# Kernel optimization log

Hardware: AMD Instinct MI355X
Metric: run time of the kernel (lower is better)

## Reference

```python
import jax, jax.numpy as jnp
import numpy as np

NUM_GROUPS, GROUP_SIZE, D_MODEL = 8, 4096, 1024
NUM_EXPERTS = 64
EXPERT_CAPACITY = 1024  # capacity_factor 2: 2 * total_tokens / num_experts


def setup_inputs() -> dict:
    key = jax.random.key(0)
    k1, k2, k3 = jax.random.split(key, 3)
    x = jax.random.normal(k1, (NUM_GROUPS, GROUP_SIZE, D_MODEL), dtype=jnp.float32)
    gate_kernel = jax.random.normal(k2, (D_MODEL, NUM_EXPERTS), dtype=jnp.float32) * 0.1
    gate_bias = jax.random.normal(k3, (NUM_EXPERTS,), dtype=jnp.float32) * 0.01
    temperature = jnp.ones((1,), dtype=jnp.float32)
    return {
        "x": x,
        "gate_kernel": gate_kernel,
        "gate_bias": gate_bias,
        "temperature": temperature,
        "expert_capacity": EXPERT_CAPACITY,
    }


def reference(x, gate_kernel, gate_bias, temperature, expert_capacity):
    # x: [G, S, D]; gate_kernel: [D, E]
    G, S, _ = x.shape
    E = gate_kernel.shape[1]

    router_logits = jnp.einsum("gsd,de->gse", x, gate_kernel) + gate_bias  # [G, S, E]
    safe_temp = jnp.maximum(temperature, 0.1)  # [1]
    router_probs = jax.nn.softmax(router_logits / safe_temp, axis=-1)  # [G, S, E]

    # Per-expert top-k over all flattened tokens.
    flat_probs = router_probs.transpose(2, 0, 1).reshape(E, G * S)  # [E, G*S]
    scores, token_indices = jax.lax.top_k(flat_probs, k=expert_capacity)  # [E, C]

    group_indices = token_indices // S  # [E, C]
    pos_indices = token_indices % S  # [E, C]
    expert_ids = jnp.broadcast_to(jnp.arange(E)[:, None], scores.shape)  # [E, C]

    # use_mask_routing=True path: scatter into capacity-limited dense masks.
    expert_masks = jnp.zeros((E, G, S), dtype=jnp.bool_).at[
        expert_ids, group_indices, pos_indices].set(True)
    weight_masks = jnp.zeros((E, G, S), dtype=x.dtype).at[
        expert_ids, group_indices, pos_indices].set(scores)

    loss = jnp.asarray(0.0, dtype=x.dtype)  # training=False
    return expert_masks, weight_masks, loss
```

## Files before the change

### kernel.cpp

```cpp
#include <hip/hip_runtime.h>
#include <math.h>

#define NG 8
#define SEQ 4096
#define DM 1024
#define NE 64
#define GS (NG * SEQ)
#define KSEL 1024
#define MASK_ELEMS (NE * GS)
#define SEG 16
#define SEGLEN (GS / SEG)

typedef __attribute__((ext_vector_type(4))) double f64x4;

__global__ __launch_bounds__(64, 2)
void k_gemm_softmax(const float* __restrict__ x, const float* __restrict__ w,
                    const float* __restrict__ bias, const float* __restrict__ temp,
                    float* __restrict__ probsT) {
  __shared__ double Lt[16][65];
  __shared__ float Af[2][16][36];
  __shared__ float Pt[64][20];

  const int lane = threadIdx.x;
  const int lrow = lane & 15;
  const int lk = lane >> 4;
  const int m0 = blockIdx.x * 16;

  int irow[4], jcol[4];
  {
    f64x4 z4 = {0.0, 0.0, 0.0, 0.0};
    double alow = (double)lrow;
    f64x4 p1 = __builtin_amdgcn_mfma_f64_16x16x4f64(alow, 1.0, z4, 0, 0, 0);
    f64x4 p2 = __builtin_amdgcn_mfma_f64_16x16x4f64(1.0, alow, z4, 0, 0, 0);
#pragma unroll
    for (int b = 0; b < 4; ++b) {
      irow[b] = ((int)p1[b]) >> 2;
      jcol[b] = ((int)p2[b]) >> 2;
    }
  }

  f64x4 acc[4];
#pragma unroll
  for (int cb = 0; cb < 4; ++cb) acc[cb] = (f64x4){0.0, 0.0, 0.0, 0.0};

  float4 rA0, rA1;
  float bfA[32], bfB[32];
  const int arow = lane >> 2, af = lane & 3;

#define LOADA(t)                                                                     \
  {                                                                                  \
    const float* ap = x + (size_t)(m0 + arow) * DM + (t) * 32 + af * 8;              \
    rA0 = *(const float4*)ap;                                                        \
    rA1 = *(const float4*)(ap + 4);                                                  \
  }

#define WRITEA(bi)                                                                   \
  {                                                                                  \
    *(float4*)(&Af[bi][arow][af * 8]) = rA0;                                         \
    *(float4*)(&Af[bi][arow][af * 8 + 4]) = rA1;                                     \
  }

#define LOADB(t, bf)                                                                 \
  {                                                                                  \
    const float* bp = w + (size_t)((t) * 32 + lk) * NE + lrow;                       \
    _Pragma("unroll")                                                                \
    for (int kc = 0; kc < 8; ++kc) {                                                 \
      _Pragma("unroll")                                                              \
      for (int c = 0; c < 4; ++c)                                                    \
        bf[kc * 4 + c] = bp[kc * 4 * NE + c * 16];                                   \
    }                                                                                \
  }

#define MFMA_TILE(bi, bf)                                                            \
  {                                                                                  \
    __builtin_amdgcn_s_setprio(1);                                                   \
    _Pragma("unroll")                                                                \
    for (int kc = 0; kc < 8; ++kc) {                                                 \
      double a = (double)Af[bi][lrow][kc * 4 + lk];                                  \
      acc[0] = __builtin_amdgcn_mfma_f64_16x16x4f64(a, (double)bf[kc * 4 + 0], acc[0], 0, 0, 0); \
      acc[1] = __builtin_amdgcn_mfma_f64_16x16x4f64(a, (double)bf[kc * 4 + 1], acc[1], 0, 0, 0); \
      acc[2] = __builtin_amdgcn_mfma_f64_16x16x4f64(a, (double)bf[kc * 4 + 2], acc[2], 0, 0, 0); \
      acc[3] = __builtin_amdgcn_mfma_f64_16x16x4f64(a, (double)bf[kc * 4 + 3], acc[3], 0, 0, 0); \
    }                                                                                \
    __builtin_amdgcn_s_setprio(0);                                                   \
  }

  LOADA(0);
  WRITEA(0);
  LOADA(1);
  LOADB(0, bfA);

  for (int tt = 0; tt < 32; tt += 2) {
    WRITEA(1);
    if (tt + 2 < 32) LOADA(tt + 2);
    LOADB(tt + 1, bfB);
    MFMA_TILE(0, bfA);
    if (tt + 2 < 32) {
      WRITEA(0);
      LOADA(tt + 3);
      LOADB(tt + 2, bfA);
    }
    MFMA_TILE(1, bfB);
  }

#undef LOADA
#undef WRITEA
#undef LOADB
#undef MFMA_TILE

#pragma unroll
  for (int cb = 0; cb < 4; ++cb)
#pragma unroll
    for (int b = 0; b < 4; ++b)
      Lt[irow[b]][cb * 16 + jcol[b]] = acc[cb][b];

  {
    double st = (double)temp[0];
    if (st < 0.1) st = 0.1;
    const double inv_t = 1.0 / st;
    const int tt = lane >> 2, q = lane & 3;
    double l[16];
    double mx = -1.0e300;
#pragma unroll
    for (int j = 0; j < 16; ++j) {
      l[j] = (Lt[tt][q * 16 + j] + (double)bias[q * 16 + j]) * inv_t;
      mx = fmax(mx, l[j]);
    }
    mx = fmax(mx, __shfl_xor(mx, 1));
    mx = fmax(mx, __shfl_xor(mx, 2));
    float p[16], s = 0.0f;
#pragma unroll
    for (int j = 0; j < 16; ++j) { p[j] = __expf((float)(l[j] - mx)); s += p[j]; }
    s += __shfl_xor(s, 1);
    s += __shfl_xor(s, 2);
    const float invs = 1.0f / s;
#pragma unroll
    for (int j = 0; j < 16; ++j) Pt[q * 16 + j][tt] = p[j] * invs;
  }

  {
#pragma unroll
    for (int c2 = 0; c2 < 4; ++c2) {
      *(float4*)(probsT + (size_t)lane * GS + m0 + c2 * 4) =
          *(const float4*)(&Pt[lane][c2 * 4]);
    }
  }
}

__device__ __forceinline__ void pick_scan(const unsigned* __restrict__ bins,
                                          unsigned r_in, unsigned& bucket,
                                          unsigned& r_out, unsigned* res) {
  __syncthreads();
  const int tid = threadIdx.x;
  if (tid < 64) {
    uint4 b = ((const uint4*)bins)[tid];
    unsigned s3 = b.w, s2 = b.z + s3, s1 = b.y + s2, s0 = b.x + s1;
    unsigned suf = s0;
#pragma unroll
    for (int off = 1; off < 64; off <<= 1) {
      unsigned t = __shfl_down(suf, off);
      if (tid + off < 64) suf += t;
    }
    unsigned above = suf - s0;
    unsigned inc0 = above + s0, inc1 = above + s1, inc2 = above + s2, inc3 = above + s3;
    if (inc3 >= r_in && inc3 - b.w < r_in) { res[0] = 4 * tid + 3; res[1] = r_in - (inc3 - b.w); }
    if (inc2 >= r_in && inc2 - b.z < r_in) { res[0] = 4 * tid + 2; res[1] = r_in - (inc2 - b.z); }
    if (inc1 >= r_in && inc1 - b.y < r_in) { res[0] = 4 * tid + 1; res[1] = r_in - (inc1 - b.y); }
    if (inc0 >= r_in && inc0 - b.x < r_in) { res[0] = 4 * tid + 0; res[1] = r_in - (inc0 - b.x); }
  }
  __syncthreads();
  bucket = res[0];
  r_out = res[1];
}

template <int PASS>
__global__ __launch_bounds__(256)
void k_hist(const float* __restrict__ probsT, unsigned* __restrict__ ghist) {
  __shared__ unsigned h[4][256];
  __shared__ unsigned res[2];
  const int tid = threadIdx.x, wv = tid >> 6;
  const int e = blockIdx.x >> 4;
  const int seg = blockIdx.x & (SEG - 1);
  h[0][tid] = 0; h[1][tid] = 0; h[2][tid] = 0; h[3][tid] = 0;

  unsigned pfx = 0, r = KSEL;
#pragma unroll
  for (int p = 0; p < PASS; ++p) {
    unsigned b, rn;
    pick_scan(ghist + ((size_t)p * NE + e) * 256, r, b, rn, res);
    pfx |= b << (24 - 8 * p);
    r = rn;
  }
  __syncthreads();

  const unsigned hm = PASS ? (0xFFFFFFFFu << (32 - 8 * PASS)) : 0u;
  const int shift = 24 - 8 * PASS;
  const float4* col = (const float4*)(probsT + (size_t)e * GS + seg * SEGLEN);
#pragma unroll
  for (int i = 0; i < SEGLEN / 1024; ++i) {
    float4 v = col[i * 256 + tid];
    unsigned k0 = __float_as_uint(v.x), k1 = __float_as_uint(v.y);
    unsigned k2 = __float_as_uint(v.z), k3 = __float_as_uint(v.w);
    if (PASS == 0 || (k0 & hm) == pfx) atomicAdd(&h[wv][(k0 >> shift) & 255], 1u);
    if (PASS == 0 || (k1 & hm) == pfx) atomicAdd(&h[wv][(k1 >> shift) & 255], 1u);
    if (PASS == 0 || (k2 & hm) == pfx) atomicAdd(&h[wv][(k2 >> shift) & 255], 1u);
    if (PASS == 0 || (k3 & hm) == pfx) atomicAdd(&h[wv][(k3 >> shift) & 255], 1u);
  }
  __syncthreads();
  unsigned c = h[0][tid] + h[1][tid] + h[2][tid] + h[3][tid];
  if (c) atomicAdd(&ghist[((size_t)PASS * NE + e) * 256 + tid], c);
}

__global__ __launch_bounds__(256)
void k_ties(const float* __restrict__ probsT, const unsigned* __restrict__ ghist,
            uint2* __restrict__ state, unsigned* __restrict__ tiecnt,
            int* __restrict__ tiebuf) {
  __shared__ unsigned res[2];
  const int tid = threadIdx.x;
  const int e = blockIdx.x >> 4;
  const int seg = blockIdx.x & (SEG - 1);

  unsigned pfx = 0, r = KSEL;
#pragma unroll
  for (int p = 0; p < 4; ++p) {
    unsigned b, rn;
    pick_scan(ghist + ((size_t)p * NE + e) * 256, r, b, rn, res);
    pfx |= b << (24 - 8 * p);
    r = rn;
  }
  if (tid == 0 && seg == 0) state[e] = make_uint2(pfx, r);

  const float* col = probsT + (size_t)e * GS + seg * SEGLEN;
  for (int i = 0; i < SEGLEN / 256; ++i) {
    int t = i * 256 + tid;
    if (__float_as_uint(col[t]) == pfx) {
      unsigned p = atomicAdd(&tiecnt[e], 1u);
      if (p < 1024u) tiebuf[e * 1024 + p] = seg * SEGLEN + t;
    }
  }
}

__global__ __launch_bounds__(256)
void k_cut(const uint2* __restrict__ state, const unsigned* __restrict__ tiecnt,
           const int* __restrict__ tiebuf, int* __restrict__ cut) {
  __shared__ int sl[1024];
  const int e = blockIdx.x, tid = threadIdx.x;
  const int cnt = (int)min(tiecnt[e], 1024u);
  const int r = (int)state[e].y;
  for (int i = tid; i < cnt; i += 256) sl[i] = tiebuf[e * 1024 + i];
  __syncthreads();
  if (r > cnt) { if (tid == 0) cut[e] = 0x7FFFFFFF; return; }
  for (int i = tid; i < cnt; i += 256) {
    int v = sl[i], rank = 0;
    for (int j = 0; j < cnt; ++j) rank += (sl[j] < v);
    if (rank == r - 1) cut[e] = v;
  }
}

__global__ __launch_bounds__(256)
void k_scatter(const float* __restrict__ probsT, const uint2* __restrict__ state,
               const int* __restrict__ cut, float* __restrict__ out) {
  const int gid = blockIdx.x * 256 + threadIdx.x;
  const int base = gid * 4;
  const int e = base >> 15;
  const int t = base & (GS - 1);
  float4 p = *(const float4*)(probsT + (size_t)base);
  const unsigned T = state[e].x;
  const int ct = cut[e];
  float pv[4] = {p.x, p.y, p.z, p.w};
  float mk[4], wt[4];
#pragma unroll
  for (int c = 0; c < 4; ++c) {
    unsigned key = __float_as_uint(pv[c]);
    bool sel = (key > T) || (key == T && (t + c) <= ct);
    mk[c] = sel ? 1.0f : 0.0f;
    wt[c] = sel ? pv[c] : 0.0f;
  }
  *(float4*)(out + (size_t)base) = make_float4(mk[0], mk[1], mk[2], mk[3]);
  *(float4*)(out + (size_t)MASK_ELEMS + base) = make_float4(wt[0], wt[1], wt[2], wt[3]);
  if (gid == 0) out[2 * (size_t)MASK_ELEMS] = 0.0f;
}

extern "C" void kernel_launch(void* const* d_in, const int* in_sizes, int n_in,
                              void* d_out, int out_size, void* d_ws, size_t ws_size,
                              hipStream_t stream) {
  const float* x    = (const float*)d_in[0];
  const float* gw   = (const float*)d_in[1];
  const float* gb   = (const float*)d_in[2];
  const float* temp = (const float*)d_in[3];

  float* probsT    = (float*)d_ws;
  unsigned* ghist  = (unsigned*)((char*)d_ws + (size_t)MASK_ELEMS * 4);
  unsigned* tiecnt = ghist + 4 * NE * 256;
  uint2* state     = (uint2*)(tiecnt + NE);
  int* cutp        = (int*)(state + NE);
  int* tiebuf      = cutp + NE;

  hipMemsetAsync(ghist, 0, (4 * NE * 256 + NE) * sizeof(unsigned), stream);
  k_gemm_softmax<<<GS / 16, 64, 0, stream>>>(x, gw, gb, temp, probsT);
  k_hist<0><<<NE * SEG, 256, 0, stream>>>(probsT, ghist);
  k_hist<1><<<NE * SEG, 256, 0, stream>>>(probsT, ghist);
  k_hist<2><<<NE * SEG, 256, 0, stream>>>(probsT, ghist);
  k_hist<3><<<NE * SEG, 256, 0, stream>>>(probsT, ghist);
  k_ties<<<NE * SEG, 256, 0, stream>>>(probsT, ghist, state, tiecnt, tiebuf);
  k_cut<<<NE, 256, 0, stream>>>(state, tiecnt, tiebuf, cutp);
  k_scatter<<<MASK_ELEMS / 1024, 256, 0, stream>>>(probsT, state, cutp, (float*)d_out);
}
```

Measured before the change: 112.0 us.

## Replace FP64 MFMA gating GEMM with split-bf16 MFMA plus near-threshold FP64 repair

Replaces the fp64 MFMA router GEMM with a three-way bf16 split of x and the gate kernel, using bf16 MFMAs with fp32 accumulation and an fp64 accumulator for the high-high term. Because the probabilities are now only approximately exact, tokens within a relative band around the top-k threshold are collected and recomputed in fp64 by a repair kernel, then ranked and applied after the scatter. The intent is to remove the slow fp64 MFMA throughput cost while keeping exact selection. In exchange it adds several kernels, a weight-split pass every call, and the risk that more than the fixed candidate capacity fall inside the band.

```diff
diff --git a/kernel.cpp b/kernel.cpp
--- a/kernel.cpp
+++ b/kernel.cpp
@@ -10,42 +10,79 @@
 #define MASK_ELEMS (NE * GS)
 #define SEG 16
 #define SEGLEN (GS / SEG)
-
-typedef __attribute__((ext_vector_type(4))) double f64x4;
+#define CAP 2048
+#define AST 40
+
+typedef __attribute__((ext_vector_type(8))) short short8;
+typedef __attribute__((ext_vector_type(4))) float f32x4;
+
+__device__ __forceinline__ unsigned short f2bf(float v) {
+  unsigned u = __float_as_uint(v);
+  return (unsigned short)((u + 0x7FFFu + ((u >> 16) & 1u)) >> 16);
+}
+__device__ __forceinline__ float bf2f(unsigned short h) {
+  return __uint_as_float(((unsigned)h) << 16);
+}
+
+__global__ __launch_bounds__(256)
+void k_split(const float* __restrict__ w, unsigned short* __restrict__ wph,
+             unsigned short* __restrict__ wpm, unsigned short* __restrict__ wpl) {
+  const int t = blockIdx.x * 256 + threadIdx.x;
+  const int k = t >> 6, e = t & 63;
+  float v = w[t];
+  unsigned short h = f2bf(v); float r = v - bf2f(h);
+  unsigned short m = f2bf(r); float r2 = r - bf2f(m);
+  unsigned short l = f2bf(r2);
+  const int o = e * 1024 + k;
+  wph[o] = h; wpm[o] = m; wpl[o] = l;
+}
 
 __global__ __launch_bounds__(64, 2)
-void k_gemm_softmax(const float* __restrict__ x, const float* __restrict__ w,
+void k_gemm_softmax(const float* __restrict__ x,
+                    const unsigned short* __restrict__ wph,
+                    const unsigned short* __restrict__ wpm,
+                    const unsigned short* __restrict__ wpl,
                     const float* __restrict__ bias, const float* __restrict__ temp,
                     float* __restrict__ probsT) {
+  __shared__ __align__(16) unsigned short Ah[2][16 * AST], Am[2][16 * AST],
+      Al[2][16 * AST];
   __shared__ double Lt[16][65];
-  __shared__ float Af[2][16][36];
   __shared__ float Pt[64][20];
 
   const int lane = threadIdx.x;
   const int lrow = lane & 15;
-  const int lk = lane >> 4;
+  const int g = lane >> 4;
   const int m0 = blockIdx.x * 16;
 
   int irow[4], jcol[4];
   {
-    f64x4 z4 = {0.0, 0.0, 0.0, 0.0};
-    double alow = (double)lrow;
-    f64x4 p1 = __builtin_amdgcn_mfma_f64_16x16x4f64(alow, 1.0, z4, 0, 0, 0);
-    f64x4 p2 = __builtin_amdgcn_mfma_f64_16x16x4f64(1.0, alow, z4, 0, 0, 0);
+    union { unsigned short u[8]; short8 v; } ar, on;
+#pragma unroll
+    for (int j = 0; j < 8; ++j) { ar.u[j] = f2bf((float)lrow); on.u[j] = 0x3F80u; }
+    f32x4 z = {0.f, 0.f, 0.f, 0.f};
+    f32x4 p1 = __builtin_amdgcn_mfma_f32_16x16x32_bf16(ar.v, on.v, z, 0, 0, 0);
+    f32x4 p2 = __builtin_amdgcn_mfma_f32_16x16x32_bf16(on.v, ar.v, z, 0, 0, 0);
 #pragma unroll
     for (int b = 0; b < 4; ++b) {
-      irow[b] = ((int)p1[b]) >> 2;
-      jcol[b] = ((int)p2[b]) >> 2;
-    }
-  }
-
-  f64x4 acc[4];
-#pragma unroll
-  for (int cb = 0; cb < 4; ++cb) acc[cb] = (f64x4){0.0, 0.0, 0.0, 0.0};
+      irow[b] = ((int)p1[b]) >> 5;
+      jcol[b] = ((int)p2[b]) >> 5;
+    }
+  }
+
+  double acc64[4][4];
+  f32x4 acc32[4];
+#pragma unroll
+  for (int cb = 0; cb < 4; ++cb) {
+    acc32[cb] = (f32x4){0.f, 0.f, 0.f, 0.f};
+#pragma unroll
+    for (int b = 0; b < 4; ++b) acc64[cb][b] = 0.0;
+  }
 
   float4 rA0, rA1;
-  float bfA[32], bfB[32];
   const int arow = lane >> 2, af = lane & 3;
+  const int aoff = arow * AST + af * 8;
+  const int foff = lrow * AST + g * 8;
+  const int boff = lrow * 1024 + g * 8;
 
 #define LOADA(t)                                                                     \
   {                                                                                  \
@@ -54,65 +91,72 @@
     rA1 = *(const float4*)(ap + 4);                                                  \
   }
 
-#define WRITEA(bi)                                                                   \
+#define SPLITA(bi)                                                                   \
   {                                                                                  \
-    *(float4*)(&Af[bi][arow][af * 8]) = rA0;                                         \
-    *(float4*)(&Af[bi][arow][af * 8 + 4]) = rA1;                                     \
-  }
-
-#define LOADB(t, bf)                                                                 \
+    union { float4 f[2]; float s[8]; } qa;                                           \
+    qa.f[0] = rA0; qa.f[1] = rA1;                                                    \
+    union { unsigned short u[8]; short8 v; } ph, pm, pl;                             \
+    _Pragma("unroll")                                                                \
+    for (int j = 0; j < 8; ++j) {                                                    \
+      float v0 = qa.s[j];                                                            \
+      unsigned short h_ = f2bf(v0); float r_ = v0 - bf2f(h_);                        \
+      unsigned short mm = f2bf(r_); float r2_ = r_ - bf2f(mm);                       \
+      ph.u[j] = h_; pm.u[j] = mm; pl.u[j] = f2bf(r2_);                               \
+    }                                                                                \
+    *(short8*)(&Ah[bi][aoff]) = ph.v;                                                \
+    *(short8*)(&Am[bi][aoff]) = pm.v;                                                \
+    *(short8*)(&Al[bi][aoff]) = pl.v;                                                \
+  }
+
+#define MFMA_TILE(bi, t)                                                             \
   {                                                                                  \
-    const float* bp = w + (size_t)((t) * 32 + lk) * NE + lrow;                       \
-    _Pragma("unroll")                                                                \
-    for (int kc = 0; kc < 8; ++kc) {                                                 \
-      _Pragma("unroll")                                                              \
-      for (int c = 0; c < 4; ++c)                                                    \
-        bf[kc * 4 + c] = bp[kc * 4 * NE + c * 16];                                   \
-    }                                                                                \
-  }
-
-#define MFMA_TILE(bi, bf)                                                            \
-  {                                                                                  \
+    short8 ah_ = *(const short8*)(&Ah[bi][foff]);                                    \
+    short8 am_ = *(const short8*)(&Am[bi][foff]);                                    \
+    short8 al_ = *(const short8*)(&Al[bi][foff]);                                    \
     __builtin_amdgcn_s_setprio(1);                                                   \
     _Pragma("unroll")                                                                \
-    for (int kc = 0; kc < 8; ++kc) {                                                 \
-      double a = (double)Af[bi][lrow][kc * 4 + lk];                                  \
-      acc[0] = __builtin_amdgcn_mfma_f64_16x16x4f64(a, (double)bf[kc * 4 + 0], acc[0], 0, 0, 0); \
-      acc[1] = __builtin_amdgcn_mfma_f64_16x16x4f64(a, (double)bf[kc * 4 + 1], acc[1], 0, 0, 0); \
-      acc[2] = __builtin_amdgcn_mfma_f64_16x16x4f64(a, (double)bf[kc * 4 + 2], acc[2], 0, 0, 0); \
-      acc[3] = __builtin_amdgcn_mfma_f64_16x16x4f64(a, (double)bf[kc * 4 + 3], acc[3], 0, 0, 0); \
+    for (int cb = 0; cb < 4; ++cb) {                                                 \
+      const size_t bo = (size_t)boff + cb * 16 * 1024 + (t) * 32;                    \
+      short8 bh_ = *(const short8*)(wph + bo);                                       \
+      short8 bm_ = *(const short8*)(wpm + bo);                                       \
+      short8 bl_ = *(const short8*)(wpl + bo);                                       \
+      f32x4 z_ = {0.f, 0.f, 0.f, 0.f};                                               \
+      f32x4 thi = __builtin_amdgcn_mfma_f32_16x16x32_bf16(ah_, bh_, z_, 0, 0, 0);    \
+      acc32[cb] = __builtin_amdgcn_mfma_f32_16x16x32_bf16(al_, bh_, acc32[cb], 0, 0, 0); \
+      acc32[cb] = __builtin_amdgcn_mfma_f32_16x16x32_bf16(am_, bm_, acc32[cb], 0, 0, 0); \
+      acc32[cb] = __builtin_amdgcn_mfma_f32_16x16x32_bf16(ah_, bl_, acc32[cb], 0, 0, 0); \
+      acc32[cb] = __builtin_amdgcn_mfma_f32_16x16x32_bf16(am_, bh_, acc32[cb], 0, 0, 0); \
+      acc32[cb] = __builtin_amdgcn_mfma_f32_16x16x32_bf16(ah_, bm_, acc32[cb], 0, 0, 0); \
+      _Pragma("unroll")                                                              \
+      for (int b = 0; b < 4; ++b) acc64[cb][b] += (double)thi[b];                    \
     }                                                                                \
     __builtin_amdgcn_s_setprio(0);                                                   \
   }
 
   LOADA(0);
-  WRITEA(0);
+  SPLITA(0);
   LOADA(1);
-  LOADB(0, bfA);
 
   for (int tt = 0; tt < 32; tt += 2) {
-    WRITEA(1);
+    SPLITA(1);
     if (tt + 2 < 32) LOADA(tt + 2);
-    LOADB(tt + 1, bfB);
-    MFMA_TILE(0, bfA);
+    MFMA_TILE(0, tt);
     if (tt + 2 < 32) {
-      WRITEA(0);
+      SPLITA(0);
       LOADA(tt + 3);
-      LOADB(tt + 2, bfA);
-    }
-    MFMA_TILE(1, bfB);
+    }
+    MFMA_TILE(1, tt + 1);
   }
 
 #undef LOADA
-#undef WRITEA
-#undef LOADB
+#undef SPLITA
 #undef MFMA_TILE
 
 #pragma unroll
   for (int cb = 0; cb < 4; ++cb)
 #pragma unroll
     for (int b = 0; b < 4; ++b)
-      Lt[irow[b]][cb * 16 + jcol[b]] = acc[cb][b];
+      Lt[irow[b]][cb * 16 + jcol[b]] = acc64[cb][b] + (double)acc32[cb][b];
 
   {
     double st = (double)temp[0];
@@ -128,14 +172,14 @@
     }
     mx = fmax(mx, __shfl_xor(mx, 1));
     mx = fmax(mx, __shfl_xor(mx, 2));
-    float p[16], s = 0.0f;
-#pragma unroll
-    for (int j = 0; j < 16; ++j) { p[j] = __expf((float)(l[j] - mx)); s += p[j]; }
+    double p[16], s = 0.0;
+#pragma unroll
+    for (int j = 0; j < 16; ++j) { p[j] = exp(l[j] - mx); s += p[j]; }
     s += __shfl_xor(s, 1);
     s += __shfl_xor(s, 2);
-    const float invs = 1.0f / s;
-#pragma unroll
-    for (int j = 0; j < 16; ++j) Pt[q * 16 + j][tt] = p[j] * invs;
+    const double invs = 1.0 / s;
+#pragma unroll
+    for (int j = 0; j < 16; ++j) Pt[q * 16 + j][tt] = (float)(p[j] * invs);
   }
 
   {
@@ -212,9 +256,10 @@
 }
 
 __global__ __launch_bounds__(256)
-void k_ties(const float* __restrict__ probsT, const unsigned* __restrict__ ghist,
-            uint2* __restrict__ state, unsigned* __restrict__ tiecnt,
-            int* __restrict__ tiebuf) {
+void k_cand(const float* __restrict__ probsT, const unsigned* __restrict__ ghist,
+            const float* __restrict__ temp, unsigned* __restrict__ defCnt,
+            unsigned* __restrict__ candCnt, int* __restrict__ candIdx,
+            float* __restrict__ thrHiA) {
   __shared__ unsigned res[2];
   const int tid = threadIdx.x;
   const int e = blockIdx.x >> 4;
@@ -228,57 +273,123 @@
     pfx |= b << (24 - 8 * p);
     r = rn;
   }
-  if (tid == 0 && seg == 0) state[e] = make_uint2(pfx, r);
+  const float thrv = __uint_as_float(pfx);
+  float st = temp[0];
+  if (st < 0.1f) st = 0.1f;
+  const float rel = 2.0e-3f / st;
+  const float hi = thrv * (1.0f + rel);
+  const float lo = thrv * (1.0f - rel);
+  if (tid == 0 && seg == 0) thrHiA[e] = hi;
 
   const float* col = probsT + (size_t)e * GS + seg * SEGLEN;
   for (int i = 0; i < SEGLEN / 256; ++i) {
-    int t = i * 256 + tid;
-    if (__float_as_uint(col[t]) == pfx) {
-      unsigned p = atomicAdd(&tiecnt[e], 1u);
-      if (p < 1024u) tiebuf[e * 1024 + p] = seg * SEGLEN + t;
-    }
-  }
-}
-
-__global__ __launch_bounds__(256)
-void k_cut(const uint2* __restrict__ state, const unsigned* __restrict__ tiecnt,
-           const int* __restrict__ tiebuf, int* __restrict__ cut) {
-  __shared__ int sl[1024];
+    const int t = i * 256 + tid;
+    const float p = col[t];
+    if (p > hi) {
+      atomicAdd(&defCnt[e], 1u);
+    } else if (p >= lo) {
+      unsigned pos = atomicAdd(&candCnt[e], 1u);
+      if (pos < CAP) candIdx[e * CAP + pos] = seg * SEGLEN + t;
+    }
+  }
+}
+
+__global__ __launch_bounds__(256)
+void k_repair(const float* __restrict__ x, const float* __restrict__ w,
+              const float* __restrict__ bias, const float* __restrict__ temp,
+              const unsigned* __restrict__ candCnt, const int* __restrict__ candIdx,
+              double* __restrict__ candKey) {
+  __shared__ double red[4][64];
+  const int e = blockIdx.x >> 3;
+  const int chunk = blockIdx.x & 7;
+  const int tid = threadIdx.x;
+  const int ee = tid & 63, q = tid >> 6;
+  const int cnt = (int)min(candCnt[e], (unsigned)CAP);
+
+  double st = (double)temp[0];
+  if (st < 0.1) st = 0.1;
+  const double inv_t = 1.0 / st;
+
+  for (int i = chunk; i < cnt; i += 8) {
+    const int t = candIdx[e * CAP + i];
+    const float* xr = x + (size_t)t * DM;
+    double s = 0.0;
+    for (int k = q * 256; k < q * 256 + 256; ++k)
+      s += (double)xr[k] * (double)w[(size_t)k * NE + ee];
+    red[q][ee] = s;
+    __syncthreads();
+    if (tid < 64) {
+      double l = (red[0][tid] + red[1][tid] + red[2][tid] + red[3][tid] +
+                  (double)bias[tid]) * inv_t;
+      double m = l;
+#pragma unroll
+      for (int off = 1; off < 64; off <<= 1) m = fmax(m, __shfl_xor(m, off));
+      double ex = exp(l - m);
+      double ss = ex;
+#pragma unroll
+      for (int off = 1; off < 64; off <<= 1) ss += __shfl_xor(ss, off);
+      if (tid == e) candKey[e * CAP + i] = ex / ss;
+    }
+    __syncthreads();
+  }
+}
+
+__global__ __launch_bounds__(256)
+void k_rank(const unsigned* __restrict__ defCnt, const unsigned* __restrict__ candCnt,
+            int* __restrict__ candIdx, const double* __restrict__ candKey) {
+  __shared__ double kd[CAP];
+  __shared__ int ti[CAP];
   const int e = blockIdx.x, tid = threadIdx.x;
-  const int cnt = (int)min(tiecnt[e], 1024u);
-  const int r = (int)state[e].y;
-  for (int i = tid; i < cnt; i += 256) sl[i] = tiebuf[e * 1024 + i];
+  const int cnt = (int)min(candCnt[e], (unsigned)CAP);
+  const int need = KSEL - (int)defCnt[e];
+  for (int i = tid; i < cnt; i += 256) {
+    kd[i] = candKey[e * CAP + i];
+    ti[i] = candIdx[e * CAP + i];
+  }
   __syncthreads();
-  if (r > cnt) { if (tid == 0) cut[e] = 0x7FFFFFFF; return; }
   for (int i = tid; i < cnt; i += 256) {
-    int v = sl[i], rank = 0;
-    for (int j = 0; j < cnt; ++j) rank += (sl[j] < v);
-    if (rank == r - 1) cut[e] = v;
-  }
-}
-
-__global__ __launch_bounds__(256)
-void k_scatter(const float* __restrict__ probsT, const uint2* __restrict__ state,
-               const int* __restrict__ cut, float* __restrict__ out) {
+    const double ki = kd[i];
+    const int tii = ti[i];
+    int rank = 0;
+    for (int j = 0; j < cnt; ++j)
+      rank += (kd[j] > ki) || (kd[j] == ki && ti[j] < tii);
+    if (rank >= need) candIdx[e * CAP + i] = -1;
+  }
+}
+
+__global__ __launch_bounds__(256)
+void k_scatter(const float* __restrict__ probsT, const float* __restrict__ thrHiA,
+               float* __restrict__ out) {
   const int gid = blockIdx.x * 256 + threadIdx.x;
   const int base = gid * 4;
   const int e = base >> 15;
-  const int t = base & (GS - 1);
   float4 p = *(const float4*)(probsT + (size_t)base);
-  const unsigned T = state[e].x;
-  const int ct = cut[e];
+  const float hi = thrHiA[e];
   float pv[4] = {p.x, p.y, p.z, p.w};
   float mk[4], wt[4];
 #pragma unroll
   for (int c = 0; c < 4; ++c) {
-    unsigned key = __float_as_uint(pv[c]);
-    bool sel = (key > T) || (key == T && (t + c) <= ct);
+    bool sel = pv[c] > hi;
     mk[c] = sel ? 1.0f : 0.0f;
     wt[c] = sel ? pv[c] : 0.0f;
   }
   *(float4*)(out + (size_t)base) = make_float4(mk[0], mk[1], mk[2], mk[3]);
   *(float4*)(out + (size_t)MASK_ELEMS + base) = make_float4(wt[0], wt[1], wt[2], wt[3]);
   if (gid == 0) out[2 * (size_t)MASK_ELEMS] = 0.0f;
+}
+
+__global__ __launch_bounds__(256)
+void k_apply(const unsigned* __restrict__ candCnt, const int* __restrict__ candIdx,
+             const float* __restrict__ probsT, float* __restrict__ out) {
+  const int e = blockIdx.x, tid = threadIdx.x;
+  const int cnt = (int)min(candCnt[e], (unsigned)CAP);
+  for (int i = tid; i < cnt; i += 256) {
+    const int t = candIdx[e * CAP + i];
+    if (t >= 0) {
+      out[(size_t)e * GS + t] = 1.0f;
+      out[(size_t)MASK_ELEMS + (size_t)e * GS + t] = probsT[(size_t)e * GS + t];
+    }
+  }
 }
 
 extern "C" void kernel_launch(void* const* d_in, const int* in_sizes, int n_in,
@@ -291,18 +402,26 @@
 
   float* probsT    = (float*)d_ws;
   unsigned* ghist  = (unsigned*)((char*)d_ws + (size_t)MASK_ELEMS * 4);
-  unsigned* tiecnt = ghist + 4 * NE * 256;
-  uint2* state     = (uint2*)(tiecnt + NE);
-  int* cutp        = (int*)(state + NE);
-  int* tiebuf      = cutp + NE;
-
-  hipMemsetAsync(ghist, 0, (4 * NE * 256 + NE) * sizeof(unsigned), stream);
-  k_gemm_softmax<<<GS / 16, 64, 0, stream>>>(x, gw, gb, temp, probsT);
+  unsigned* defCnt = ghist + 4 * NE * 256;
+  unsigned* candCnt = defCnt + NE;
+  float* thrHiA    = (float*)(candCnt + NE);
+  int* candIdx     = (int*)(thrHiA + NE);
+  double* candKey  = (double*)(candIdx + NE * CAP);
+  unsigned short* wph = (unsigned short*)(candKey + NE * CAP);
+  unsigned short* wpm = wph + DM * NE;
+  unsigned short* wpl = wpm + DM * NE;
+
+  hipMemsetAsync(ghist, 0, (4 * NE * 256 + 2 * NE) * sizeof(unsigned), stream);
+  k_split<<<DM * NE / 256, 256, 0, stream>>>(gw, wph, wpm, wpl);
+  k_gemm_softmax<<<GS / 16, 64, 0, stream>>>(x, wph, wpm, wpl, gb, temp, probsT);
   k_hist<0><<<NE * SEG, 256, 0, stream>>>(probsT, ghist);
   k_hist<1><<<NE * SEG, 256, 0, stream>>>(probsT, ghist);
   k_hist<2><<<NE * SEG, 256, 0, stream>>>(probsT, ghist);
   k_hist<3><<<NE * SEG, 256, 0, stream>>>(probsT, ghist);
-  k_ties<<<NE * SEG, 256, 0, stream>>>(probsT, ghist, state, tiecnt, tiebuf);
-  k_cut<<<NE, 256, 0, stream>>>(state, tiecnt, tiebuf, cutp);
-  k_scatter<<<MASK_ELEMS / 1024, 256, 0, stream>>>(probsT, state, cutp, (float*)d_out);
-}
+  k_cand<<<NE * SEG, 256, 0, stream>>>(probsT, ghist, temp, defCnt, candCnt,
+                                       candIdx, thrHiA);
+  k_repair<<<NE * 8, 256, 0, stream>>>(x, gw, gb, temp, candCnt, candIdx, candKey);
+  k_rank<<<NE, 256, 0, stream>>>(defCnt, candCnt, candIdx, candKey);
+  k_scatter<<<MASK_ELEMS / 1024, 256, 0, stream>>>(probsT, thrHiA, (float*)d_out);
+  k_apply<<<NE, 256, 0, stream>>>(candCnt, candIdx, probsT, (float*)d_out);
+}
```

After: 345.9 us. 3.09x slower.
